# Kernel optimization log

Hardware: AMD Instinct MI355X
Metric: run time of the kernel (lower is better)

The kernel has to match this reference:

```python
import jax, jax.numpy as jnp
import numpy as np

B, T, C, H, O = 64, 256, 2048, 512, 11
THRESHOLD = 1.0
LEAK = 0.003
OUTPUT_LEAK = LEAK * 0.5


def setup_inputs() -> dict:
    key = jax.random.key(0)
    k1, k2, k3, k4 = jax.random.split(key, 4)
    x = jax.random.normal(k1, (B, T, C), dtype=jnp.float32)
    # xavier_uniform(gain=0.1) for fc1: bound = 0.1*sqrt(6/(C+H))
    b1 = 0.1 * np.sqrt(6.0 / (C + H))
    w1 = jax.random.uniform(k2, (H, C), jnp.float32, -b1, b1)
    # orthogonal(gain=0.1) for fc_rec -> approximate with small gaussian scaled like orthogonal rows
    w_rec = 0.1 * jnp.linalg.qr(jax.random.normal(k3, (H, H), jnp.float32))[0]
    b2 = 0.3 * np.sqrt(6.0 / (H + O))
    w2 = jax.random.uniform(k4, (O, H), jnp.float32, -b2, b2)
    return {"x": x, "w1": w1, "w_rec": w_rec, "w2": w2}


def reference(x, w1, w_rec, w2):
    batch, t_steps, _ = x.shape
    n_hidden = w1.shape[0]
    n_output = w2.shape[0]
    dt = x.dtype

    def step(carry, x_t):
        v1, spk1, v2, out_sum = carry
        # input + recurrent current: [B,H]
        i1 = x_t @ w1.T + spk1 @ w_rec.T
        # subtractive LIF: leak, threshold, subtractive reset
        v1 = v1 + i1 - LEAK
        spk = (v1 >= THRESHOLD).astype(dt)
        v1 = v1 - spk * THRESHOLD
        # non-spiking output accumulator neuron: [B,O]
        i2 = spk @ w2.T
        v2 = jnp.maximum(v2 + i2 - OUTPUT_LEAK, 0.0)
        out_sum = out_sum + v2
        return (v1, spk, v2, out_sum), None

    init = (
        jnp.zeros((batch, n_hidden), dt),
        jnp.zeros((batch, n_hidden), dt),
        jnp.zeros((batch, n_output), dt),
        jnp.zeros((batch, n_output), dt),
    )
    (_, _, _, out_sum), _ = jax.lax.scan(step, init, jnp.swapaxes(x, 0, 1))
    return out_sum / t_steps
```

## Files before the change

kernel.cpp:

```cpp
#include <hip/hip_runtime.h>
#include <cstddef>

#define B_ 64
#define T_ 256
#define C_ 2048
#define H_ 512
#define O_ 11
#define THRESH 1.0f
#define LEAK_ 0.003f
#define OLEAK_ 0.0015f

typedef float v2f __attribute__((ext_vector_type(2)));

__global__ __launch_bounds__(256) void transpose_wrec(const float* __restrict__ w,
                                                      float* __restrict__ wt) {
    __shared__ float tile[32][33];
    int tx = threadIdx.x, ty = threadIdx.y;
    int x = blockIdx.x * 32 + tx;
    int y = blockIdx.y * 32 + ty;
#pragma unroll
    for (int i = 0; i < 32; i += 8)
        tile[ty + i][tx] = w[(size_t)(y + i) * H_ + x];
    __syncthreads();
    int x2 = blockIdx.y * 32 + tx;
    int y2 = blockIdx.x * 32 + ty;
#pragma unroll
    for (int i = 0; i < 32; i += 8)
        wt[(size_t)(y2 + i) * H_ + x2] = tile[tx][ty + i];
}

#define BM 128
#define BN 128
#define BK 16

template <int S>
__global__ __launch_bounds__(256) void gemm_ff(const float* __restrict__ A,
                                               const float* __restrict__ Bw,
                                               float* __restrict__ Pout) {
    const int K = C_;
    const int N = H_;
    const int kLen  = C_ / S;
    const int kBase = blockIdx.z * kLen;

    __shared__ float As[BK][BM];
    __shared__ float Bs[BK][BN];

    const int t  = threadIdx.x;
    const int tx = t & 15;
    const int ty = t >> 4;
    const int lr = t >> 2;
    const int lc = (t & 3) * 4;

    const float* Aptr = A  + (size_t)(blockIdx.y * BM + lr) * K + kBase + lc;
    const float* Bptr = Bw + (size_t)(blockIdx.x * BN + lr) * K + kBase + lc;

    v2f acc[8][4];
#pragma unroll
    for (int i = 0; i < 8; ++i)
#pragma unroll
        for (int j = 0; j < 4; ++j) acc[i][j] = (v2f){0.f, 0.f};

    for (int k0 = 0; k0 < kLen; k0 += BK) {
        float4 a0 = *(const float4*)(Aptr);
        float4 a1 = *(const float4*)(Aptr + (size_t)64 * K);
        float4 b0 = *(const float4*)(Bptr);
        float4 b1 = *(const float4*)(Bptr + (size_t)64 * K);
        Aptr += BK; Bptr += BK;

        __syncthreads();
        As[lc + 0][lr] = a0.x; As[lc + 1][lr] = a0.y;
        As[lc + 2][lr] = a0.z; As[lc + 3][lr] = a0.w;
        As[lc + 0][lr + 64] = a1.x; As[lc + 1][lr + 64] = a1.y;
        As[lc + 2][lr + 64] = a1.z; As[lc + 3][lr + 64] = a1.w;
        Bs[lc + 0][lr] = b0.x; Bs[lc + 1][lr] = b0.y;
        Bs[lc + 2][lr] = b0.z; Bs[lc + 3][lr] = b0.w;
        Bs[lc + 0][lr + 64] = b1.x; Bs[lc + 1][lr + 64] = b1.y;
        Bs[lc + 2][lr + 64] = b1.z; Bs[lc + 3][lr + 64] = b1.w;
        __syncthreads();

#pragma unroll
        for (int k = 0; k < BK; ++k) {
            float4 alo = *(const float4*)&As[k][ty * 4];
            float4 ahi = *(const float4*)&As[k][64 + ty * 4];
            float4 blo = *(const float4*)&Bs[k][tx * 4];
            float4 bhi = *(const float4*)&Bs[k][64 + tx * 4];
            v2f b0v = {blo.x, blo.y}, b1v = {blo.z, blo.w};
            v2f b2v = {bhi.x, bhi.y}, b3v = {bhi.z, bhi.w};
            float av[8] = {alo.x, alo.y, alo.z, alo.w, ahi.x, ahi.y, ahi.z, ahi.w};
#pragma unroll
            for (int i = 0; i < 8; ++i) {
                v2f ai = {av[i], av[i]};
                acc[i][0] += ai * b0v;
                acc[i][1] += ai * b1v;
                acc[i][2] += ai * b2v;
                acc[i][3] += ai * b3v;
            }
        }
    }

    float* P = Pout + (size_t)blockIdx.z * ((size_t)B_ * T_ * H_);
#pragma unroll
    for (int i = 0; i < 8; ++i) {
        int row = blockIdx.y * BM + (i < 4 ? ty * 4 + i : 64 + ty * 4 + (i - 4));
        float* Cp = P + (size_t)row * N + blockIdx.x * BN;
        float4 c0 = {acc[i][0].x, acc[i][0].y, acc[i][1].x, acc[i][1].y};
        float4 c1 = {acc[i][2].x, acc[i][2].y, acc[i][3].x, acc[i][3].y};
        *(float4*)(Cp + tx * 4)      = c0;
        *(float4*)(Cp + 64 + tx * 4) = c1;
    }
}

template <int S>
__global__ __launch_bounds__(512) void snn_rec(const float* __restrict__ I1,
                                               const float* __restrict__ wrT,
                                               const float* __restrict__ w2,
                                               float* __restrict__ out) {
    const int b    = blockIdx.x;
    const int h    = threadIdx.x;
    const int lane = h & 63;
    const int w    = h >> 6;

    __shared__ float w2sT[H_ * 12];
    __shared__ int   lists[2][H_];
    __shared__ int   wcnt[8];
    __shared__ float v2s[O_];
    __shared__ float osum[O_];

    for (int k = h; k < H_; k += H_) {}
#pragma unroll
    for (int o = 0; o < O_; ++o) w2sT[h * 12 + o] = w2[o * H_ + h];
    if (h < O_) { v2s[h] = 0.f; osum[h] = 0.f; }

    float v1 = 0.f;
    int   pc = 0;
    const float*  i1p  = I1 + (size_t)b * T_ * H_ + h;
    const float*  wr_h = wrT + h;
    const size_t  PARTF = (size_t)B_ * T_ * H_;

    float pf[S];
#pragma unroll
    for (int s = 0; s < S; ++s) pf[s] = i1p[s * PARTF];
    __syncthreads();

    for (int t = 0; t < T_; ++t) {
        const int cur = t & 1;

        float acc = -LEAK_;
#pragma unroll
        for (int s = 0; s < S; ++s) acc += pf[s];

        const int tn = (t + 1 < T_) ? t + 1 : t;
#pragma unroll
        for (int s = 0; s < S; ++s) pf[s] = i1p[s * PARTF + (size_t)tn * H_];

        const int* pl = lists[cur ^ 1];
        int j = 0;
        for (; j + 7 < pc; j += 8) {
            const int4 ia = *(const int4*)(pl + j);
            const int4 ib = *(const int4*)(pl + j + 4);
            float g0 = wr_h[ia.x * H_];
            float g1 = wr_h[ia.y * H_];
            float g2 = wr_h[ia.z * H_];
            float g3 = wr_h[ia.w * H_];
            float g4 = wr_h[ib.x * H_];
            float g5 = wr_h[ib.y * H_];
            float g6 = wr_h[ib.z * H_];
            float g7 = wr_h[ib.w * H_];
            acc += g0; acc += g1; acc += g2; acc += g3;
            acc += g4; acc += g5; acc += g6; acc += g7;
        }
        for (; j < pc; ++j) acc += wr_h[pl[j] * H_];

        v1 += acc;
        const bool spike = (v1 >= THRESH);
        if (spike) v1 -= THRESH;

        unsigned long long m = __ballot(spike);
        int lb = __popcll(m & ((1ull << lane) - 1ull));
        if (lane == 0) wcnt[w] = (int)__popcll(m);
        __syncthreads();

        int base = 0, tot = 0;
#pragma unroll
        for (int ww = 0; ww < 8; ++ww) {
            int c = wcnt[ww];
            if (ww < w) base += c;
            tot += c;
        }
        if (spike) lists[cur][base + lb] = h;
        __syncthreads();

        if (h < O_) {
            const int* cl = lists[cur];
            float s = 0.f;
            for (int j2 = 0; j2 < tot; ++j2) s += w2sT[cl[j2] * 12 + h];
            float v2 = v2s[h] + s - OLEAK_;
            v2 = v2 > 0.f ? v2 : 0.f;
            v2s[h] = v2;
            osum[h] += v2;
        }
        pc = tot;
    }
    __syncthreads();
    if (h < O_) out[b * O_ + h] = osum[h] * (1.0f / (float)T_);
}

extern "C" void kernel_launch(void* const* d_in, const int* in_sizes, int n_in,
                              void* d_out, int out_size, void* d_ws, size_t ws_size,
                              hipStream_t stream) {
    const float* x     = (const float*)d_in[0];
    const float* w1    = (const float*)d_in[1];
    const float* w_rec = (const float*)d_in[2];
    const float* w2    = (const float*)d_in[3];
    float* out = (float*)d_out;

    const size_t PART = (size_t)B_ * T_ * H_ * sizeof(float);
    const size_t WRT  = (size_t)H_ * H_ * sizeof(float);

    int S = 1;
    if (ws_size >= 4 * PART + WRT) S = 4;
    else if (ws_size >= 2 * PART + WRT) S = 2;

    float* P   = (float*)d_ws;
    float* wrT = (float*)((char*)d_ws + (size_t)S * PART);

    transpose_wrec<<<dim3(H_ / 32, H_ / 32), dim3(32, 8), 0, stream>>>(w_rec, wrT);

    dim3 ggrid(H_ / BN, (B_ * T_) / BM, S);
    switch (S) {
        case 4:
            gemm_ff<4><<<ggrid, dim3(256), 0, stream>>>(x, w1, P);
            snn_rec<4><<<dim3(B_), dim3(H_), 0, stream>>>(P, wrT, w2, out);
            break;
        case 2:
            gemm_ff<2><<<ggrid, dim3(256), 0, stream>>>(x, w1, P);
            snn_rec<2><<<dim3(B_), dim3(H_), 0, stream>>>(P, wrT, w2, out);
            break;
        default:
            gemm_ff<1><<<ggrid, dim3(256), 0, stream>>>(x, w1, P);
            snn_rec<1><<<dim3(B_), dim3(H_), 0, stream>>>(P, wrT, w2, out);
            break;
    }
}
```

Before: 771.7 us.

## Enlarge GEMM tile, add split-K reduce kernel, single-wave recurrent SNN kernel

The feedforward GEMM tile grows from 128 to 256 rows per block, with padded shared memory and a two-block occupancy hint, so each thread computes a 16x8 sub-tile. Split-K partial sums are now summed by a separate elementwise reduce kernel instead of inside the recurrent kernel. The recurrent kernel is rewritten to use one 64-lane wave per batch item, with each lane owning 8 hidden neurons and spikes held as ballot bitmasks. This removes the shared-memory spike lists and block-wide barriers, at the cost of less parallelism per batch item and an extra pass over the partial-sum buffers.

```diff
diff --git a/kernel.cpp b/kernel.cpp
--- a/kernel.cpp
+++ b/kernel.cpp
@@ -29,21 +29,21 @@
         wt[(size_t)(y2 + i) * H_ + x2] = tile[tx][ty + i];
 }
 
-#define BM 128
+#define BM 256
 #define BN 128
 #define BK 16
 
 template <int S>
-__global__ __launch_bounds__(256) void gemm_ff(const float* __restrict__ A,
-                                               const float* __restrict__ Bw,
-                                               float* __restrict__ Pout) {
+__global__ __launch_bounds__(256, 2) void gemm_ff(const float* __restrict__ A,
+                                                  const float* __restrict__ Bw,
+                                                  float* __restrict__ Pout) {
     const int K = C_;
     const int N = H_;
     const int kLen  = C_ / S;
     const int kBase = blockIdx.z * kLen;
 
-    __shared__ float As[BK][BM];
-    __shared__ float Bs[BK][BN];
+    __shared__ float As[BK][BM + 4];
+    __shared__ float Bs[BK][BN + 4];
 
     const int t  = threadIdx.x;
     const int tx = t & 15;
@@ -54,41 +54,50 @@
     const float* Aptr = A  + (size_t)(blockIdx.y * BM + lr) * K + kBase + lc;
     const float* Bptr = Bw + (size_t)(blockIdx.x * BN + lr) * K + kBase + lc;
 
-    v2f acc[8][4];
-#pragma unroll
-    for (int i = 0; i < 8; ++i)
+    v2f acc[16][4];
+#pragma unroll
+    for (int i = 0; i < 16; ++i)
 #pragma unroll
         for (int j = 0; j < 4; ++j) acc[i][j] = (v2f){0.f, 0.f};
 
     for (int k0 = 0; k0 < kLen; k0 += BK) {
         float4 a0 = *(const float4*)(Aptr);
-        float4 a1 = *(const float4*)(Aptr + (size_t)64 * K);
+        float4 a1 = *(const float4*)(Aptr + (size_t)64  * K);
+        float4 a2 = *(const float4*)(Aptr + (size_t)128 * K);
+        float4 a3 = *(const float4*)(Aptr + (size_t)192 * K);
         float4 b0 = *(const float4*)(Bptr);
         float4 b1 = *(const float4*)(Bptr + (size_t)64 * K);
         Aptr += BK; Bptr += BK;
 
         __syncthreads();
-        As[lc + 0][lr] = a0.x; As[lc + 1][lr] = a0.y;
-        As[lc + 2][lr] = a0.z; As[lc + 3][lr] = a0.w;
-        As[lc + 0][lr + 64] = a1.x; As[lc + 1][lr + 64] = a1.y;
-        As[lc + 2][lr + 64] = a1.z; As[lc + 3][lr + 64] = a1.w;
-        Bs[lc + 0][lr] = b0.x; Bs[lc + 1][lr] = b0.y;
-        Bs[lc + 2][lr] = b0.z; Bs[lc + 3][lr] = b0.w;
-        Bs[lc + 0][lr + 64] = b1.x; Bs[lc + 1][lr + 64] = b1.y;
-        Bs[lc + 2][lr + 64] = b1.z; Bs[lc + 3][lr + 64] = b1.w;
+        As[lc + 0][lr]       = a0.x; As[lc + 1][lr]       = a0.y;
+        As[lc + 2][lr]       = a0.z; As[lc + 3][lr]       = a0.w;
+        As[lc + 0][lr + 64]  = a1.x; As[lc + 1][lr + 64]  = a1.y;
+        As[lc + 2][lr + 64]  = a1.z; As[lc + 3][lr + 64]  = a1.w;
+        As[lc + 0][lr + 128] = a2.x; As[lc + 1][lr + 128] = a2.y;
+        As[lc + 2][lr + 128] = a2.z; As[lc + 3][lr + 128] = a2.w;
+        As[lc + 0][lr + 192] = a3.x; As[lc + 1][lr + 192] = a3.y;
+        As[lc + 2][lr + 192] = a3.z; As[lc + 3][lr + 192] = a3.w;
+        Bs[lc + 0][lr]       = b0.x; Bs[lc + 1][lr]       = b0.y;
+        Bs[lc + 2][lr]       = b0.z; Bs[lc + 3][lr]       = b0.w;
+        Bs[lc + 0][lr + 64]  = b1.x; Bs[lc + 1][lr + 64]  = b1.y;
+        Bs[lc + 2][lr + 64]  = b1.z; Bs[lc + 3][lr + 64]  = b1.w;
         __syncthreads();
 
 #pragma unroll
         for (int k = 0; k < BK; ++k) {
-            float4 alo = *(const float4*)&As[k][ty * 4];
-            float4 ahi = *(const float4*)&As[k][64 + ty * 4];
+            float4 af0 = *(const float4*)&As[k][ty * 8];
+            float4 af1 = *(const float4*)&As[k][ty * 8 + 4];
+            float4 af2 = *(const float4*)&As[k][128 + ty * 8];
+            float4 af3 = *(const float4*)&As[k][128 + ty * 8 + 4];
             float4 blo = *(const float4*)&Bs[k][tx * 4];
             float4 bhi = *(const float4*)&Bs[k][64 + tx * 4];
             v2f b0v = {blo.x, blo.y}, b1v = {blo.z, blo.w};
             v2f b2v = {bhi.x, bhi.y}, b3v = {bhi.z, bhi.w};
-            float av[8] = {alo.x, alo.y, alo.z, alo.w, ahi.x, ahi.y, ahi.z, ahi.w};
-#pragma unroll
-            for (int i = 0; i < 8; ++i) {
+            float av[16] = {af0.x, af0.y, af0.z, af0.w, af1.x, af1.y, af1.z, af1.w,
+                            af2.x, af2.y, af2.z, af2.w, af3.x, af3.y, af3.z, af3.w};
+#pragma unroll
+            for (int i = 0; i < 16; ++i) {
                 v2f ai = {av[i], av[i]};
                 acc[i][0] += ai * b0v;
                 acc[i][1] += ai * b1v;
@@ -100,8 +109,8 @@
 
     float* P = Pout + (size_t)blockIdx.z * ((size_t)B_ * T_ * H_);
 #pragma unroll
-    for (int i = 0; i < 8; ++i) {
-        int row = blockIdx.y * BM + (i < 4 ? ty * 4 + i : 64 + ty * 4 + (i - 4));
+    for (int i = 0; i < 16; ++i) {
+        int row = blockIdx.y * BM + (i < 8 ? ty * 8 + i : 128 + ty * 8 + (i - 8));
         float* Cp = P + (size_t)row * N + blockIdx.x * BN;
         float4 c0 = {acc[i][0].x, acc[i][0].y, acc[i][1].x, acc[i][1].y};
         float4 c1 = {acc[i][2].x, acc[i][2].y, acc[i][3].x, acc[i][3].y};
@@ -111,98 +120,82 @@
 }
 
 template <int S>
-__global__ __launch_bounds__(512) void snn_rec(const float* __restrict__ I1,
-                                               const float* __restrict__ wrT,
-                                               const float* __restrict__ w2,
-                                               float* __restrict__ out) {
-    const int b    = blockIdx.x;
-    const int h    = threadIdx.x;
-    const int lane = h & 63;
-    const int w    = h >> 6;
-
-    __shared__ float w2sT[H_ * 12];
-    __shared__ int   lists[2][H_];
-    __shared__ int   wcnt[8];
-    __shared__ float v2s[O_];
-    __shared__ float osum[O_];
-
-    for (int k = h; k < H_; k += H_) {}
-#pragma unroll
-    for (int o = 0; o < O_; ++o) w2sT[h * 12 + o] = w2[o * H_ + h];
-    if (h < O_) { v2s[h] = 0.f; osum[h] = 0.f; }
-
-    float v1 = 0.f;
-    int   pc = 0;
-    const float*  i1p  = I1 + (size_t)b * T_ * H_ + h;
-    const float*  wr_h = wrT + h;
-    const size_t  PARTF = (size_t)B_ * T_ * H_;
-
-    float pf[S];
-#pragma unroll
-    for (int s = 0; s < S; ++s) pf[s] = i1p[s * PARTF];
-    __syncthreads();
+__global__ __launch_bounds__(256) void reduce_parts(float* __restrict__ P) {
+    const size_t n = (size_t)B_ * T_ * H_;
+    size_t i = ((size_t)blockIdx.x * 256 + threadIdx.x) * 4;
+    if (i >= n) return;
+    float4 a = *(float4*)(P + i);
+#pragma unroll
+    for (int s = 1; s < S; ++s) {
+        float4 bq = *(const float4*)(P + (size_t)s * n + i);
+        a.x += bq.x; a.y += bq.y; a.z += bq.z; a.w += bq.w;
+    }
+    *(float4*)(P + i) = a;
+}
+
+__global__ __launch_bounds__(64) void snn_rec(const float* __restrict__ I1,
+                                              const float* __restrict__ wrT,
+                                              const float* __restrict__ w2,
+                                              float* __restrict__ out) {
+    const int b = blockIdx.x;
+    const int L = threadIdx.x;
+
+    const float* i1p = I1 + (size_t)b * T_ * H_ + L;
+    const float* wrL = wrT + L;
+    const float* w2L = w2 + (size_t)(L < O_ ? L : 0) * H_;
+
+    float v1[8], pf[8];
+    unsigned long long masks[8];
+#pragma unroll
+    for (int r = 0; r < 8; ++r) { v1[r] = 0.f; masks[r] = 0ull; pf[r] = i1p[r * 64]; }
+    float v2 = 0.f, osum = 0.f;
 
     for (int t = 0; t < T_; ++t) {
-        const int cur = t & 1;
-
-        float acc = -LEAK_;
-#pragma unroll
-        for (int s = 0; s < S; ++s) acc += pf[s];
-
-        const int tn = (t + 1 < T_) ? t + 1 : t;
-#pragma unroll
-        for (int s = 0; s < S; ++s) pf[s] = i1p[s * PARTF + (size_t)tn * H_];
-
-        const int* pl = lists[cur ^ 1];
-        int j = 0;
-        for (; j + 7 < pc; j += 8) {
-            const int4 ia = *(const int4*)(pl + j);
-            const int4 ib = *(const int4*)(pl + j + 4);
-            float g0 = wr_h[ia.x * H_];
-            float g1 = wr_h[ia.y * H_];
-            float g2 = wr_h[ia.z * H_];
-            float g3 = wr_h[ia.w * H_];
-            float g4 = wr_h[ib.x * H_];
-            float g5 = wr_h[ib.y * H_];
-            float g6 = wr_h[ib.z * H_];
-            float g7 = wr_h[ib.w * H_];
-            acc += g0; acc += g1; acc += g2; acc += g3;
-            acc += g4; acc += g5; acc += g6; acc += g7;
-        }
-        for (; j < pc; ++j) acc += wr_h[pl[j] * H_];
-
-        v1 += acc;
-        const bool spike = (v1 >= THRESH);
-        if (spike) v1 -= THRESH;
-
-        unsigned long long m = __ballot(spike);
-        int lb = __popcll(m & ((1ull << lane) - 1ull));
-        if (lane == 0) wcnt[w] = (int)__popcll(m);
-        __syncthreads();
-
-        int base = 0, tot = 0;
-#pragma unroll
-        for (int ww = 0; ww < 8; ++ww) {
-            int c = wcnt[ww];
-            if (ww < w) base += c;
-            tot += c;
-        }
-        if (spike) lists[cur][base + lb] = h;
-        __syncthreads();
-
-        if (h < O_) {
-            const int* cl = lists[cur];
-            float s = 0.f;
-            for (int j2 = 0; j2 < tot; ++j2) s += w2sT[cl[j2] * 12 + h];
-            float v2 = v2s[h] + s - OLEAK_;
-            v2 = v2 > 0.f ? v2 : 0.f;
-            v2s[h] = v2;
-            osum[h] += v2;
-        }
-        pc = tot;
-    }
-    __syncthreads();
-    if (h < O_) out[b * O_ + h] = osum[h] * (1.0f / (float)T_);
+        float acc[8];
+#pragma unroll
+        for (int r = 0; r < 8; ++r) acc[r] = pf[r] - LEAK_;
+
+        const float* nx = i1p + (size_t)((t + 1 < T_) ? t + 1 : t) * H_;
+#pragma unroll
+        for (int r = 0; r < 8; ++r) pf[r] = nx[r * 64];
+
+#pragma unroll
+        for (int r2 = 0; r2 < 8; ++r2) {
+            unsigned long long m = masks[r2];
+            while (m) {
+                int j = (r2 << 6) + __builtin_ctzll(m);
+                m &= (m - 1);
+                const float* wj = wrL + (size_t)j * H_;
+#pragma unroll
+                for (int r = 0; r < 8; ++r) acc[r] += wj[r * 64];
+            }
+        }
+
+#pragma unroll
+        for (int r = 0; r < 8; ++r) v1[r] += acc[r];
+#pragma unroll
+        for (int r = 0; r < 8; ++r) {
+            masks[r] = __ballot(v1[r] >= THRESH);
+            if (v1[r] >= THRESH) v1[r] -= THRESH;
+        }
+
+        float s = 0.f;
+        if (L < O_) {
+#pragma unroll
+            for (int r2 = 0; r2 < 8; ++r2) {
+                unsigned long long m = masks[r2];
+                while (m) {
+                    int j = (r2 << 6) + __builtin_ctzll(m);
+                    m &= (m - 1);
+                    s += w2L[j];
+                }
+            }
+        }
+        v2 = v2 + s - OLEAK_;
+        v2 = v2 > 0.f ? v2 : 0.f;
+        osum += v2;
+    }
+    if (L < O_) out[b * O_ + L] = osum * (1.0f / (float)T_);
 }
 
 extern "C" void kernel_launch(void* const* d_in, const int* in_sizes, int n_in,
@@ -227,18 +220,19 @@
     transpose_wrec<<<dim3(H_ / 32, H_ / 32), dim3(32, 8), 0, stream>>>(w_rec, wrT);
 
     dim3 ggrid(H_ / BN, (B_ * T_) / BM, S);
+    const int rblocks = (int)(((size_t)B_ * T_ * H_ / 4 + 255) / 256);
     switch (S) {
         case 4:
             gemm_ff<4><<<ggrid, dim3(256), 0, stream>>>(x, w1, P);
-            snn_rec<4><<<dim3(B_), dim3(H_), 0, stream>>>(P, wrT, w2, out);
+            reduce_parts<4><<<dim3(rblocks), dim3(256), 0, stream>>>(P);
             break;
         case 2:
             gemm_ff<2><<<ggrid, dim3(256), 0, stream>>>(x, w1, P);
-            snn_rec<2><<<dim3(B_), dim3(H_), 0, stream>>>(P, wrT, w2, out);
+            reduce_parts<2><<<dim3(rblocks), dim3(256), 0, stream>>>(P);
             break;
         default:
             gemm_ff<1><<<ggrid, dim3(256), 0, stream>>>(x, w1, P);
-            snn_rec<1><<<dim3(B_), dim3(H_), 0, stream>>>(P, wrT, w2, out);
             break;
     }
-}
+    snn_rec<<<dim3(B_), dim3(64), 0, stream>>>(P, wrT, w2, out);
+}
```

Result: no change. 777.5 us (+0.8%).
